# Optimization experiments

Hardware: AMD Instinct MI355X
Metric: run time of the kernel (lower is better)

The kernel has to match this reference:

```python
import jax, jax.numpy as jnp
import numpy as np

M_DIM = 1024
N_HEADS = 16
H_DIM = M_DIM // N_HEADS
FFN_H = 2 * M_DIM
B, S = 2, 2048
EPS = 1e-5
NEG = -1e9


def layernorm(x, g, b):
    mu = jnp.mean(x, axis=-1, keepdims=True)
    var = jnp.mean((x - mu) ** 2, axis=-1, keepdims=True)
    return (x - mu) * jax.lax.rsqrt(var + EPS) * g + b


def setup_inputs() -> dict:
    key = jax.random.key(0)
    ks = jax.random.split(key, 16)
    sc = 0.02
    return {
        "x": jax.random.normal(ks[0], (B, S, M_DIM), jnp.float32),
        "attention_mask": jnp.ones((B, S), jnp.int32),
        # per-head QKV projections stacked over heads: [H, M, D]
        "Wq": jax.random.normal(ks[1], (N_HEADS, M_DIM, H_DIM), jnp.float32) * sc,
        "bq": jnp.zeros((N_HEADS, H_DIM), jnp.float32),
        "Wk": jax.random.normal(ks[2], (N_HEADS, M_DIM, H_DIM), jnp.float32) * sc,
        "bk": jnp.zeros((N_HEADS, H_DIM), jnp.float32),
        "Wv": jax.random.normal(ks[3], (N_HEADS, M_DIM, H_DIM), jnp.float32) * sc,
        "bv": jnp.zeros((N_HEADS, H_DIM), jnp.float32),
        "Wo": jax.random.normal(ks[4], (M_DIM, M_DIM), jnp.float32) * sc,
        "bo": jnp.zeros((M_DIM,), jnp.float32),
        "g1": jnp.ones((M_DIM,), jnp.float32),
        "b1": jnp.zeros((M_DIM,), jnp.float32),
        "W1": jax.random.normal(ks[5], (M_DIM, FFN_H), jnp.float32) * sc,
        "bias1": jnp.zeros((FFN_H,), jnp.float32),
        "W2": jax.random.normal(ks[6], (FFN_H, M_DIM), jnp.float32) * sc,
        "bias2": jnp.zeros((M_DIM,), jnp.float32),
        "g2": jnp.ones((M_DIM,), jnp.float32),
        "b2": jnp.zeros((M_DIM,), jnp.float32),
    }


def reference(x, attention_mask, Wq, bq, Wk, bk, Wv, bv, Wo, bo, g1, b1, W1, bias1, W2, bias2, g2, b2):
    # All heads at once (the torch code loops over heads; same math).
    q = jnp.einsum("bsm,hmd->bhsd", x, Wq) + bq[None, :, None, :]
    k = jnp.einsum("bsm,hmd->bhsd", x, Wk) + bk[None, :, None, :]
    v = jnp.einsum("bsm,hmd->bhsd", x, Wv) + bv[None, :, None, :]
    scores = jnp.einsum("bhqd,bhkd->bhqk", q, k) / jnp.sqrt(jnp.float32(H_DIM))
    mask = attention_mask[:, None, None, :].astype(bool)  # [B,1,1,S] over keys
    scores = jnp.where(mask, scores, NEG)
    attn = jax.nn.softmax(scores, axis=-1)
    ctx = jnp.einsum("bhqk,bhkd->bhqd", attn, v)
    ctx = ctx.transpose(0, 2, 1, 3).reshape(x.shape[0], x.shape[1], M_DIM)  # concat heads
    out = ctx @ Wo + bo
    out = layernorm(out + x, g1, b1)
    fout = jax.nn.relu(out @ W1 + bias1) @ W2 + bias2
    out = layernorm(out + fout, g2, b2)
    return out
```

## Files before the change

### kernel.cpp

```cpp
#include <hip/hip_runtime.h>

#define MDIM 1024
#define FFH  2048
#define SEQ  2048
#define AST  72
#define VST  136
#define QSCL 0.18033688f

#if __has_builtin(__builtin_amdgcn_exp2f)
  #define EXP2(x) __builtin_amdgcn_exp2f(x)
#else
  #define EXP2(x) exp2f(x)
#endif

typedef __attribute__((ext_vector_type(8))) __bf16 bf16x8;
typedef __attribute__((ext_vector_type(4))) float floatx4;
typedef __attribute__((ext_vector_type(8))) unsigned short ushort8;
typedef __attribute__((address_space(3))) unsigned int lds_uint;
typedef const __attribute__((address_space(1))) unsigned int g_uint;

__device__ __forceinline__ unsigned short f2bf(float f){
  union { float f; unsigned u; } v; v.f = f;
  unsigned u = v.u;
  u += 0x7fffu + ((u >> 16) & 1u);
  return (unsigned short)(u >> 16);
}
__device__ __forceinline__ unsigned short f2bf_tr(float f){
  union { float f; unsigned u; } v; v.f = f;
  return (unsigned short)(v.u >> 16);
}

__global__ void k_cvt_qb(const float* __restrict__ x, unsigned short* __restrict__ xb,
                         const float* __restrict__ bq, const float* __restrict__ bk,
                         const float* __restrict__ bv, float* __restrict__ qbias){
  const int bid = blockIdx.x, t = threadIdx.x;
  if (bid < 4096){
    int i = (bid * 256 + t) * 4;
    float4 v = *(const float4*)(x + i);
    ushort4 o;
    o.x = f2bf(v.x); o.y = f2bf(v.y); o.z = f2bf(v.z); o.w = f2bf(v.w);
    *(ushort4*)(xb + i) = o;
  } else {
    int i = (bid - 4096) * 256 + t;
    qbias[i] = (i < 1024) ? bq[i] * QSCL : (i < 2048) ? bk[i - 1024] : bv[i - 2048];
  }
}

__global__ void __launch_bounds__(256) k_prep_w(const float* __restrict__ Wo, const float* __restrict__ W1,
                                                const float* __restrict__ W2, const float* __restrict__ Wq,
                                                const float* __restrict__ Wk, const float* __restrict__ Wv,
                                                unsigned short* __restrict__ wot, unsigned short* __restrict__ w1t,
                                                unsigned short* __restrict__ w2t, unsigned short* __restrict__ wqkvt){
  __shared__ unsigned short Ts[32 * 36];
  const int t = threadIdx.x, bid = blockIdx.x;
  const int lr = t >> 3, lc4 = (t & 7) << 2;
  if (bid >= 5120){
    const int id = bid - 5120;
    const int xm = id & 31, yd = (id >> 5) & 1, z = id >> 6;
    const int tensor = z >> 4, h = z & 15;
    const float* W = (tensor == 0) ? Wq : (tensor == 1) ? Wk : Wv;
    const float scl = (tensor == 0) ? QSCL : 1.0f;
    const int m0 = xm << 5, d0 = yd << 5;
    float4 v = *(const float4*)(W + ((size_t)h << 16) + (size_t)(m0 + lr) * 64 + d0 + lc4);
    ushort4 o; o.x = f2bf(v.x * scl); o.y = f2bf(v.y * scl); o.z = f2bf(v.z * scl); o.w = f2bf(v.w * scl);
    *(ushort4*)&Ts[lr * 36 + lc4] = o;
    __syncthreads();
    ushort4 w;
    w.x = Ts[(lc4 + 0) * 36 + lr];
    w.y = Ts[(lc4 + 1) * 36 + lr];
    w.z = Ts[(lc4 + 2) * 36 + lr];
    w.w = Ts[(lc4 + 3) * 36 + lr];
    const int n = (tensor << 10) + (h << 6) + d0 + lr;
    *(ushort4*)(wqkvt + ((size_t)n << 10) + m0 + lc4) = w;
    return;
  }
  const float* src; unsigned short* dst; int K, N, k0, n0;
  if (bid < 1024){
    src = Wo; dst = wot; K = 1024; N = 1024;
    n0 = (bid & 31) << 5; k0 = (bid >> 5) << 5;
  } else if (bid < 3072){
    const int id = bid - 1024;
    src = W1; dst = w1t; K = 1024; N = 2048;
    n0 = (id & 63) << 5; k0 = (id >> 6) << 5;
  } else {
    const int id = bid - 3072;
    src = W2; dst = w2t; K = 2048; N = 1024;
    n0 = (id & 31) << 5; k0 = (id >> 5) << 5;
  }
  float4 v = *(const float4*)(src + (size_t)(k0 + lr) * N + n0 + lc4);
  ushort4 o; o.x = f2bf(v.x); o.y = f2bf(v.y); o.z = f2bf(v.z); o.w = f2bf(v.w);
  *(ushort4*)&Ts[lr * 36 + lc4] = o;
  __syncthreads();
  ushort4 w;
  w.x = Ts[(lc4 + 0) * 36 + lr];
  w.y = Ts[(lc4 + 1) * 36 + lr];
  w.z = Ts[(lc4 + 2) * 36 + lr];
  w.w = Ts[(lc4 + 3) * 36 + lr];
  *(ushort4*)(dst + (size_t)(n0 + lr) * K + k0 + lc4) = w;
}

template<int RELU, int OUTBF>
__global__ void __launch_bounds__(256) k_gemm128(const unsigned short* __restrict__ A,
                                                 const unsigned short* __restrict__ Bt,
                                                 const float* __restrict__ bias,
                                                 void* __restrict__ Cout, int N, int K){
  __shared__ unsigned short As[2 * 128 * 32];
  __shared__ unsigned short Bs[2 * 128 * 32];
  const int t = threadIdx.x;
  const int m0 = blockIdx.y << 7, n0 = blockIdx.x << 7;
  const int lane = t & 63, w = t >> 6;
  const int quad = lane >> 4, l16 = lane & 15;
  const int mw = (w & 1) << 6, nw = (w >> 1) << 6;
  floatx4 acc[4][4];
  #pragma unroll
  for (int i = 0; i < 4; i++)
    #pragma unroll
    for (int j = 0; j < 4; j++) acc[i][j] = (floatx4){0.f, 0.f, 0.f, 0.f};
  const unsigned short* Ag  = A  + (size_t)(m0 + (t >> 2)) * K + ((t & 3) << 3);
  const unsigned short* Ag2 = Ag + (size_t)64 * K;
  const unsigned short* Bg  = Bt + (size_t)(n0 + (t >> 2)) * K + ((t & 3) << 3);
  const unsigned short* Bg2 = Bg + (size_t)64 * K;
  for (int kb = 0; kb < K; kb += 64){
    #pragma unroll
    for (int s = 0; s < 2; s++){
      const int ko = kb + (s << 5), lo = (s << 12) + (t << 3);
      __builtin_amdgcn_global_load_lds((g_uint*)(Ag  + ko), (lds_uint*)&As[lo],        16, 0, 0);
      __builtin_amdgcn_global_load_lds((g_uint*)(Ag2 + ko), (lds_uint*)&As[lo + 2048], 16, 0, 0);
      __builtin_amdgcn_global_load_lds((g_uint*)(Bg  + ko), (lds_uint*)&Bs[lo],        16, 0, 0);
      __builtin_amdgcn_global_load_lds((g_uint*)(Bg2 + ko), (lds_uint*)&Bs[lo + 2048], 16, 0, 0);
    }
    __syncthreads();
    #pragma unroll
    for (int s = 0; s < 2; s++){
      const int sb = s << 12;
      bf16x8 af[4], bf[4];
      #pragma unroll
      for (int mt = 0; mt < 4; mt++)
        af[mt] = *(const bf16x8*)&As[sb + ((mw + (mt << 4) + l16) << 5) + (quad << 3)];
      #pragma unroll
      for (int nt = 0; nt < 4; nt++)
        bf[nt] = *(const bf16x8*)&Bs[sb + ((nw + (nt << 4) + l16) << 5) + (quad << 3)];
      #pragma unroll
      for (int mt = 0; mt < 4; mt++)
        #pragma unroll
        for (int nt = 0; nt < 4; nt++)
          acc[mt][nt] = __builtin_amdgcn_mfma_f32_16x16x32_bf16(af[mt], bf[nt], acc[mt][nt], 0, 0, 0);
    }
    __syncthreads();
  }
  #pragma unroll
  for (int nt = 0; nt < 4; nt++){
    const int col = n0 + nw + (nt << 4) + l16;
    const float bsv = bias[col];
    #pragma unroll
    for (int mt = 0; mt < 4; mt++){
      const int row = m0 + mw + (mt << 4) + (quad << 2);
      #pragma unroll
      for (int r = 0; r < 4; r++){
        float v = acc[mt][nt][r] + bsv;
        if (RELU) v = fmaxf(v, 0.f);
        if (OUTBF) ((unsigned short*)Cout)[(size_t)(row + r) * N + col] = f2bf(v);
        else       ((float*)Cout)[(size_t)(row + r) * N + col] = v;
      }
    }
  }
}

template<int RELU, int OUTBF>
__global__ void __launch_bounds__(256) k_gemm64n(const unsigned short* __restrict__ A,
                                                 const unsigned short* __restrict__ Bt,
                                                 const float* __restrict__ bias,
                                                 void* __restrict__ Cout, int N, int K){
  __shared__ unsigned short As[2 * 128 * 32];
  __shared__ unsigned short Bs[2 * 64 * 32];
  const int t = threadIdx.x;
  const int m0 = blockIdx.y << 7, n0 = blockIdx.x << 6;
  const int lane = t & 63, w = t >> 6;
  const int quad = lane >> 4, l16 = lane & 15;
  const int mw = (w & 1) << 6, nw = (w >> 1) << 5;
  floatx4 acc[4][2];
  #pragma unroll
  for (int i = 0; i < 4; i++)
    #pragma unroll
    for (int j = 0; j < 2; j++) acc[i][j] = (floatx4){0.f, 0.f, 0.f, 0.f};
  const unsigned short* Ag  = A  + (size_t)(m0 + (t >> 2)) * K + ((t & 3) << 3);
  const unsigned short* Ag2 = Ag + (size_t)64 * K;
  const unsigned short* Bg  = Bt + (size_t)(n0 + (t >> 2)) * K + ((t & 3) << 3);
  for (int kb = 0; kb < K; kb += 64){
    #pragma unroll
    for (int s = 0; s < 2; s++){
      const int ko = kb + (s << 5);
      __builtin_amdgcn_global_load_lds((g_uint*)(Ag  + ko), (lds_uint*)&As[(s << 12) + (t << 3)],        16, 0, 0);
      __builtin_amdgcn_global_load_lds((g_uint*)(Ag2 + ko), (lds_uint*)&As[(s << 12) + (t << 3) + 2048], 16, 0, 0);
      __builtin_amdgcn_global_load_lds((g_uint*)(Bg  + ko), (lds_uint*)&Bs[(s << 11) + (t << 3)],        16, 0, 0);
    }
    __syncthreads();
    #pragma unroll
    for (int s = 0; s < 2; s++){
      bf16x8 af[4], bf[2];
      #pragma unroll
      for (int mt = 0; mt < 4; mt++)
        af[mt] = *(const bf16x8*)&As[(s << 12) + ((mw + (mt << 4) + l16) << 5) + (quad << 3)];
      #pragma unroll
      for (int nt = 0; nt < 2; nt++)
        bf[nt] = *(const bf16x8*)&Bs[(s << 11) + ((nw + (nt << 4) + l16) << 5) + (quad << 3)];
      #pragma unroll
      for (int mt = 0; mt < 4; mt++)
        #pragma unroll
        for (int nt = 0; nt < 2; nt++)
          acc[mt][nt] = __builtin_amdgcn_mfma_f32_16x16x32_bf16(af[mt], bf[nt], acc[mt][nt], 0, 0, 0);
    }
    __syncthreads();
  }
  #pragma unroll
  for (int nt = 0; nt < 2; nt++){
    const int col = n0 + nw + (nt << 4) + l16;
    const float bsv = bias[col];
    #pragma unroll
    for (int mt = 0; mt < 4; mt++){
      const int row = m0 + mw + (mt << 4) + (quad << 2);
      #pragma unroll
      for (int r = 0; r < 4; r++){
        float v = acc[mt][nt][r] + bsv;
        if (RELU) v = fmaxf(v, 0.f);
        if (OUTBF) ((unsigned short*)Cout)[(size_t)(row + r) * N + col] = f2bf(v);
        else       ((float*)Cout)[(size_t)(row + r) * N + col] = v;
      }
    }
  }
}

__global__ void __launch_bounds__(256, 2) k_attn(const unsigned short* __restrict__ qkvb,
                                                 const int* __restrict__ amask,
                                                 unsigned short* __restrict__ ctxb){
  __shared__ __align__(16) unsigned short Ks[2][128 * AST];
  __shared__ __align__(16) unsigned short Vt[2][64 * VST];
  __shared__ __align__(16) int msk[2][128];
  const int t = threadIdx.x;
  const int w = t >> 6, lane = t & 63;
  const int quad = lane >> 4, l16 = lane & 15;
  const int b = blockIdx.y >> 4, h = blockIdx.y & 15;
  const int q0 = blockIdx.x << 7;
  const int r0 = (w << 5) + l16;
  const int r1 = r0 + 16;
  const int sr = t >> 2, sc = (t & 3) << 4;
  const int kg = t >> 4, dc = (t & 15) << 2;
  const int swz  = (dc >> 4) & 3;
  const int pc0  = ((((kg & 3) | ((kg >> 3) << 2)) ^ swz) << 3) | (((kg >> 2) & 1) << 2);

  {
    const int qr = t >> 1, qc = (t & 1) << 5;
    const unsigned short* qs = qkvb + (size_t)((b << 11) + q0 + qr) * 3072 + (h << 6) + qc;
    unsigned short* qd = &Ks[0][qr * AST + qc];
    *(uint4*)(qd)      = *(const uint4*)(qs);
    *(uint4*)(qd + 8)  = *(const uint4*)(qs + 8);
    *(uint4*)(qd + 16) = *(const uint4*)(qs + 16);
    *(uint4*)(qd + 24) = *(const uint4*)(qs + 24);
  }
  __syncthreads();
  const bf16x8 qa0 = *(const bf16x8*)&Ks[0][r0 * AST + (quad << 3)];
  const bf16x8 qa1 = *(const bf16x8*)&Ks[0][r0 * AST + (quad << 3) + 32];
  const bf16x8 qb0 = *(const bf16x8*)&Ks[0][r1 * AST + (quad << 3)];
  const bf16x8 qb1 = *(const bf16x8*)&Ks[0][r1 * AST + (quad << 3) + 32];

  floatx4 accA[4], accB[4];
  #pragma unroll
  for (int i = 0; i < 4; i++){
    accA[i] = (floatx4){0.f, 0.f, 0.f, 0.f};
    accB[i] = (floatx4){0.f, 0.f, 0.f, 0.f};
  }
  float l_runA = 0.f, l_runB = 0.f;

  const unsigned short* kbase  = qkvb + (size_t)((b << 11) + sr) * 3072 + 1024 + (h << 6) + sc;
  const unsigned short* kbase2 = kbase + (size_t)64 * 3072;
  const unsigned short* vbase  = qkvb + (size_t)((b << 11) + (kg << 2)) * 3072 + 2048 + (h << 6) + dc;
  const unsigned short* vbase2 = vbase + (size_t)64 * 3072;
  const int* mbase = amask + (b << 11);

  uint4 krA, krB, krC, krD;
  ushort4 va0, va1, va2, va3, vb0, vb1, vb2, vb3;
  int mreg = 1;

#define LOADT(tt) { \
    const size_t off = (size_t)((tt) << 7) * 3072; \
    krA = *(const uint4*)(kbase + off); \
    krB = *(const uint4*)(kbase + off + 8); \
    krC = *(const uint4*)(kbase2 + off); \
    krD = *(const uint4*)(kbase2 + off + 8); \
    va0 = *(const ushort4*)(vbase + off); \
    va1 = *(const ushort4*)(vbase + off + 3072); \
    va2 = *(const ushort4*)(vbase + off + 2 * 3072); \
    va3 = *(const ushort4*)(vbase + off + 3 * 3072); \
    vb0 = *(const ushort4*)(vbase2 + off); \
    vb1 = *(const ushort4*)(vbase2 + off + 3072); \
    vb2 = *(const ushort4*)(vbase2 + off + 2 * 3072); \
    vb3 = *(const ushort4*)(vbase2 + off + 3 * 3072); \
    if (t < 128) mreg = mbase[((tt) << 7) + t]; \
  }

#define STORET(dst) { \
    unsigned short* Kd = Ks[dst]; \
    unsigned short* Vd = Vt[dst]; \
    *(uint4*)&Kd[sr * AST + sc]            = krA; \
    *(uint4*)&Kd[sr * AST + sc + 8]        = krB; \
    *(uint4*)&Kd[(sr + 64) * AST + sc]     = krC; \
    *(uint4*)&Kd[(sr + 64) * AST + sc + 8] = krD; \
    ushort4 cc; \
    cc.x = va0.x; cc.y = va1.x; cc.z = va2.x; cc.w = va3.x; *(ushort4*)&Vd[(dc + 0) * VST + pc0] = cc; \
    cc.x = va0.y; cc.y = va1.y; cc.z = va2.y; cc.w = va3.y; *(ushort4*)&Vd[(dc + 1) * VST + pc0] = cc; \
    cc.x = va0.z; cc.y = va1.z; cc.z = va2.z; cc.w = va3.z; *(ushort4*)&Vd[(dc + 2) * VST + pc0] = cc; \
    cc.x = va0.w; cc.y = va1.w; cc.z = va2.w; cc.w = va3.w; *(ushort4*)&Vd[(dc + 3) * VST + pc0] = cc; \
    cc.x = vb0.x; cc.y = vb1.x; cc.z = vb2.x; cc.w = vb3.x; *(ushort4*)&Vd[(dc + 0) * VST + pc0 + 64] = cc; \
    cc.x = vb0.y; cc.y = vb1.y; cc.z = vb2.y; cc.w = vb3.y; *(ushort4*)&Vd[(dc + 1) * VST + pc0 + 64] = cc; \
    cc.x = vb0.z; cc.y = vb1.z; cc.z = vb2.z; cc.w = vb3.z; *(ushort4*)&Vd[(dc + 2) * VST + pc0 + 64] = cc; \
    cc.x = vb0.w; cc.y = vb1.w; cc.z = vb2.w; cc.w = vb3.w; *(ushort4*)&Vd[(dc + 3) * VST + pc0 + 64] = cc; \
    if (t < 128) msk[dst][t] = mreg; \
  }

  LOADT(0);
  __syncthreads();
  STORET(0);
  LOADT(1);
  __syncthreads();

  int c = 0;
  for (int kt = 0; kt < 16; kt++){
    if (kt + 1 < 16) STORET(c ^ 1);
    if (kt + 2 < 16) LOADT(kt + 2);
    {
      const unsigned short* Kc = Ks[c];
      const unsigned short* Vc = Vt[c];
      const int* Mc = msk[c];
      float lsA = 0.f, lsB = 0.f;
      #pragma unroll
      for (int s = 0; s < 4; s++){
        const unsigned short* kp = &Kc[((s << 5) + l16) * AST + (quad << 3)];
        const bf16x8 k00 = *(const bf16x8*)(kp);
        const bf16x8 k01 = *(const bf16x8*)(kp + 32);
        const bf16x8 k10 = *(const bf16x8*)(kp + (AST << 4));
        const bf16x8 k11 = *(const bf16x8*)(kp + (AST << 4) + 32);
        floatx4 sA0 = (floatx4){0.f, 0.f, 0.f, 0.f};
        floatx4 sB0 = (floatx4){0.f, 0.f, 0.f, 0.f};
        floatx4 sA1 = (floatx4){0.f, 0.f, 0.f, 0.f};
        floatx4 sB1 = (floatx4){0.f, 0.f, 0.f, 0.f};
        __builtin_amdgcn_s_setprio(1);
        sA0 = __builtin_amdgcn_mfma_f32_16x16x32_bf16(k00, qa0, sA0, 0, 0, 0);
        sA0 = __builtin_amdgcn_mfma_f32_16x16x32_bf16(k01, qa1, sA0, 0, 0, 0);
        sB0 = __builtin_amdgcn_mfma_f32_16x16x32_bf16(k00, qb0, sB0, 0, 0, 0);
        sB0 = __builtin_amdgcn_mfma_f32_16x16x32_bf16(k01, qb1, sB0, 0, 0, 0);
        sA1 = __builtin_amdgcn_mfma_f32_16x16x32_bf16(k10, qa0, sA1, 0, 0, 0);
        sA1 = __builtin_amdgcn_mfma_f32_16x16x32_bf16(k11, qa1, sA1, 0, 0, 0);
        sB1 = __builtin_amdgcn_mfma_f32_16x16x32_bf16(k10, qb0, sB1, 0, 0, 0);
        sB1 = __builtin_amdgcn_mfma_f32_16x16x32_bf16(k11, qb1, sB1, 0, 0, 0);
        __builtin_amdgcn_s_setprio(0);
        const int4 m0 = *(const int4*)&Mc[(s << 5) + (quad << 2)];
        const int4 m1 = *(const int4*)&Mc[(s << 5) + 16 + (quad << 2)];
        const float a0 = m0.x ? EXP2(sA0[0]) : 0.f;
        const float a1 = m0.y ? EXP2(sA0[1]) : 0.f;
        const float a2 = m0.z ? EXP2(sA0[2]) : 0.f;
        const float a3 = m0.w ? EXP2(sA0[3]) : 0.f;
        const float a4 = m1.x ? EXP2(sA1[0]) : 0.f;
        const float a5 = m1.y ? EXP2(sA1[1]) : 0.f;
        const float a6 = m1.z ? EXP2(sA1[2]) : 0.f;
        const float a7 = m1.w ? EXP2(sA1[3]) : 0.f;
        const float b0 = m0.x ? EXP2(sB0[0]) : 0.f;
        const float b1 = m0.y ? EXP2(sB0[1]) : 0.f;
        const float b2 = m0.z ? EXP2(sB0[2]) : 0.f;
        const float b3 = m0.w ? EXP2(sB0[3]) : 0.f;
        const float b4 = m1.x ? EXP2(sB1[0]) : 0.f;
        const float b5 = m1.y ? EXP2(sB1[1]) : 0.f;
        const float b6 = m1.z ? EXP2(sB1[2]) : 0.f;
        const float b7 = m1.w ? EXP2(sB1[3]) : 0.f;
        lsA += (a0 + a1) + (a2 + a3) + (a4 + a5) + (a6 + a7);
        lsB += (b0 + b1) + (b2 + b3) + (b4 + b5) + (b6 + b7);
        ushort8 uA, uB;
        uA[0] = f2bf_tr(a0); uA[1] = f2bf_tr(a1); uA[2] = f2bf_tr(a2); uA[3] = f2bf_tr(a3);
        uA[4] = f2bf_tr(a4); uA[5] = f2bf_tr(a5); uA[6] = f2bf_tr(a6); uA[7] = f2bf_tr(a7);
        uB[0] = f2bf_tr(b0); uB[1] = f2bf_tr(b1); uB[2] = f2bf_tr(b2); uB[3] = f2bf_tr(b3);
        uB[4] = f2bf_tr(b4); uB[5] = f2bf_tr(b5); uB[6] = f2bf_tr(b6); uB[7] = f2bf_tr(b7);
        const bf16x8 pfA = __builtin_bit_cast(bf16x8, uA);
        const bf16x8 pfB = __builtin_bit_cast(bf16x8, uB);
        __builtin_amdgcn_s_setprio(1);
        #pragma unroll
        for (int mt = 0; mt < 4; mt++){
          const bf16x8 vf = *(const bf16x8*)&Vc[((mt << 4) + l16) * VST + ((((s << 2) + quad) ^ mt) << 3)];
          accA[mt] = __builtin_amdgcn_mfma_f32_16x16x32_bf16(vf, pfA, accA[mt], 0, 0, 0);
          accB[mt] = __builtin_amdgcn_mfma_f32_16x16x32_bf16(vf, pfB, accB[mt], 0, 0, 0);
        }
        __builtin_amdgcn_s_setprio(0);
      }
      l_runA += lsA;
      l_runB += lsB;
    }
    __syncthreads();
    c ^= 1;
  }
#undef LOADT
#undef STORET

  l_runA += __shfl_xor(l_runA, 16);
  l_runA += __shfl_xor(l_runA, 32);
  l_runB += __shfl_xor(l_runB, 16);
  l_runB += __shfl_xor(l_runB, 32);
  const float liA = 1.f / l_runA;
  const float liB = 1.f / l_runB;
  unsigned short* oA = ctxb + (size_t)((b << 11) + q0 + r0) * 1024 + (h << 6);
  unsigned short* oB = ctxb + (size_t)((b << 11) + q0 + r1) * 1024 + (h << 6);
  #pragma unroll
  for (int mt = 0; mt < 4; mt++){
    ushort4 o;
    o.x = f2bf(accA[mt][0] * liA);
    o.y = f2bf(accA[mt][1] * liA);
    o.z = f2bf(accA[mt][2] * liA);
    o.w = f2bf(accA[mt][3] * liA);
    *(ushort4*)&oA[(mt << 4) + (quad << 2)] = o;
    o.x = f2bf(accB[mt][0] * liB);
    o.y = f2bf(accB[mt][1] * liB);
    o.z = f2bf(accB[mt][2] * liB);
    o.w = f2bf(accB[mt][3] * liB);
    *(ushort4*)&oB[(mt << 4) + (quad << 2)] = o;
  }
}

__global__ void __launch_bounds__(256) k_ln(const unsigned short* __restrict__ a,
                                            const float* __restrict__ res,
                                            const float* __restrict__ gg, const float* __restrict__ bb,
                                            float* __restrict__ out, unsigned short* __restrict__ outb){
  const int row = blockIdx.x, t = threadIdx.x;
  const ushort4 au = ((const ushort4*)(a + (size_t)row * 1024))[t];
  const float4 rv = ((const float4*)(res + (size_t)row * 1024))[t];
  float4 v;
  { union { unsigned u; float f; } c;
    c.u = (unsigned)au.x << 16; v.x = c.f + rv.x;
    c.u = (unsigned)au.y << 16; v.y = c.f + rv.y;
    c.u = (unsigned)au.z << 16; v.z = c.f + rv.z;
    c.u = (unsigned)au.w << 16; v.w = c.f + rv.w; }
  float sum = v.x + v.y + v.z + v.w;
  float ss  = v.x * v.x + v.y * v.y + v.z * v.z + v.w * v.w;
  #pragma unroll
  for (int off = 32; off > 0; off >>= 1){
    sum += __shfl_down(sum, off);
    ss  += __shfl_down(ss, off);
  }
  __shared__ float red[8];
  const int w = t >> 6;
  if ((t & 63) == 0){ red[w] = sum; red[4 + w] = ss; }
  __syncthreads();
  const float S  = red[0] + red[1] + red[2] + red[3];
  const float SS = red[4] + red[5] + red[6] + red[7];
  const float mu  = S * (1.f / 1024.f);
  const float var = SS * (1.f / 1024.f) - mu * mu;
  const float rs  = rsqrtf(var + 1e-5f);
  const float4 gv = ((const float4*)gg)[t];
  const float4 bv = ((const float4*)bb)[t];
  float4 o;
  o.x = (v.x - mu) * rs * gv.x + bv.x;
  o.y = (v.y - mu) * rs * gv.y + bv.y;
  o.z = (v.z - mu) * rs * gv.z + bv.z;
  o.w = (v.w - mu) * rs * gv.w + bv.w;
  ((float4*)(out + (size_t)row * 1024))[t] = o;
  if (outb){
    ushort4 ob; ob.x = f2bf(o.x); ob.y = f2bf(o.y); ob.z = f2bf(o.z); ob.w = f2bf(o.w);
    ((ushort4*)(outb + (size_t)row * 1024))[t] = ob;
  }
}

extern "C" void kernel_launch(void* const* d_in, const int* in_sizes, int n_in,
                              void* d_out, int out_size, void* d_ws, size_t ws_size,
                              hipStream_t stream){
  const float* x     = (const float*)d_in[0];
  const int*   amask = (const int*)d_in[1];
  const float* Wq    = (const float*)d_in[2];
  const float* bq    = (const float*)d_in[3];
  const float* Wk    = (const float*)d_in[4];
  const float* bk    = (const float*)d_in[5];
  const float* Wv    = (const float*)d_in[6];
  const float* bv    = (const float*)d_in[7];
  const float* Wo    = (const float*)d_in[8];
  const float* bo    = (const float*)d_in[9];
  const float* g1    = (const float*)d_in[10];
  const float* b1    = (const float*)d_in[11];
  const float* W1    = (const float*)d_in[12];
  const float* bias1 = (const float*)d_in[13];
  const float* W2    = (const float*)d_in[14];
  const float* bias2 = (const float*)d_in[15];
  const float* g2    = (const float*)d_in[16];
  const float* b2    = (const float*)d_in[17];

  char* ws = (char*)d_ws;
  unsigned short* xb    = (unsigned short*)(ws + 0);
  unsigned short* wqkvt = (unsigned short*)(ws + 8388608);
  float*          qbias = (float*)         (ws + 14680064);
  unsigned short* wot   = (unsigned short*)(ws + 14692352);
  unsigned short* w1t   = (unsigned short*)(ws + 16789504);
  unsigned short* w2t   = (unsigned short*)(ws + 20983808);
  unsigned short* ctxb  = (unsigned short*)(ws + 25178112);
  unsigned short* attnb = (unsigned short*)(ws + 33566720);
  unsigned short* fbufb = attnb;
  unsigned short* qkvb  = (unsigned short*)(ws + 50343936);
  float*          out1  = (float*)         (ws + 50343936);
  unsigned short* out1b = (unsigned short*)(ws + 50343936 + 25165824);
  unsigned short* h1    = (unsigned short*)(ws + 50343936 + 33554432);

  k_cvt_qb<<<dim3(4108), dim3(256), 0, stream>>>(x, xb, bq, bk, bv, qbias);
  k_prep_w<<<dim3(8192), dim3(256), 0, stream>>>(Wo, W1, W2, Wq, Wk, Wv, wot, w1t, w2t, wqkvt);

  k_gemm128<0,1><<<dim3(24, 32), dim3(256), 0, stream>>>(xb, wqkvt, qbias, qkvb, 3072, 1024);
  k_attn<<<dim3(16, 32), dim3(256), 0, stream>>>(qkvb, amask, ctxb);
  k_gemm64n<0,1><<<dim3(16, 32), dim3(256), 0, stream>>>(ctxb, wot, bo, attnb, MDIM, 1024);
  k_ln<<<dim3(4096), dim3(256), 0, stream>>>(attnb, x, g1, b1, out1, out1b);
  k_gemm128<1,1><<<dim3(16, 32), dim3(256), 0, stream>>>(out1b, w1t, bias1, h1, FFH, 1024);
  k_gemm64n<0,1><<<dim3(16, 32), dim3(256), 0, stream>>>(h1, w2t, bias2, fbufb, MDIM, 2048);
  k_ln<<<dim3(4096), dim3(256), 0, stream>>>(fbufb, out1, g2, b2, (float*)d_out, nullptr);
}
```

Baseline: 312.6 us.

## Double-buffer LDS tiles in bf16 GEMM kernels to overlap loads with MFMA

Both GEMM kernels (128x128 and 128x64 tiles) now use two LDS buffers. The next K-tile's global_load_lds is issued into the spare buffer before the MFMA work on the current buffer, with one barrier per iteration. The aim is to hide global-to-LDS latency behind matrix math instead of stalling on it each step. In exchange, per-block LDS use doubles, which can cut the number of resident blocks per CU.

```diff
diff --git a/kernel.cpp b/kernel.cpp
--- a/kernel.cpp
+++ b/kernel.cpp
@@ -104,8 +104,8 @@
                                                  const unsigned short* __restrict__ Bt,
                                                  const float* __restrict__ bias,
                                                  void* __restrict__ Cout, int N, int K){
-  __shared__ unsigned short As[2 * 128 * 32];
-  __shared__ unsigned short Bs[2 * 128 * 32];
+  __shared__ unsigned short As[2][2 * 128 * 32];
+  __shared__ unsigned short Bs[2][2 * 128 * 32];
   const int t = threadIdx.x;
   const int m0 = blockIdx.y << 7, n0 = blockIdx.x << 7;
   const int lane = t & 63, w = t >> 6;
@@ -120,26 +120,34 @@
   const unsigned short* Ag2 = Ag + (size_t)64 * K;
   const unsigned short* Bg  = Bt + (size_t)(n0 + (t >> 2)) * K + ((t & 3) << 3);
   const unsigned short* Bg2 = Bg + (size_t)64 * K;
+
+#define STG128(Ad, Bd, kb) { \
+    _Pragma("unroll") \
+    for (int s = 0; s < 2; s++){ \
+      const int ko = (kb) + (s << 5), lo = (s << 12) + (t << 3); \
+      __builtin_amdgcn_global_load_lds((g_uint*)(Ag  + ko), (lds_uint*)&(Ad)[lo],        16, 0, 0); \
+      __builtin_amdgcn_global_load_lds((g_uint*)(Ag2 + ko), (lds_uint*)&(Ad)[lo + 2048], 16, 0, 0); \
+      __builtin_amdgcn_global_load_lds((g_uint*)(Bg  + ko), (lds_uint*)&(Bd)[lo],        16, 0, 0); \
+      __builtin_amdgcn_global_load_lds((g_uint*)(Bg2 + ko), (lds_uint*)&(Bd)[lo + 2048], 16, 0, 0); \
+    } }
+
+  STG128(As[0], Bs[0], 0);
+  __syncthreads();
+  int cur = 0;
   for (int kb = 0; kb < K; kb += 64){
-    #pragma unroll
-    for (int s = 0; s < 2; s++){
-      const int ko = kb + (s << 5), lo = (s << 12) + (t << 3);
-      __builtin_amdgcn_global_load_lds((g_uint*)(Ag  + ko), (lds_uint*)&As[lo],        16, 0, 0);
-      __builtin_amdgcn_global_load_lds((g_uint*)(Ag2 + ko), (lds_uint*)&As[lo + 2048], 16, 0, 0);
-      __builtin_amdgcn_global_load_lds((g_uint*)(Bg  + ko), (lds_uint*)&Bs[lo],        16, 0, 0);
-      __builtin_amdgcn_global_load_lds((g_uint*)(Bg2 + ko), (lds_uint*)&Bs[lo + 2048], 16, 0, 0);
-    }
-    __syncthreads();
+    if (kb + 64 < K) STG128(As[cur ^ 1], Bs[cur ^ 1], kb + 64);
+    const unsigned short* Ar = As[cur];
+    const unsigned short* Br = Bs[cur];
     #pragma unroll
     for (int s = 0; s < 2; s++){
       const int sb = s << 12;
       bf16x8 af[4], bf[4];
       #pragma unroll
       for (int mt = 0; mt < 4; mt++)
-        af[mt] = *(const bf16x8*)&As[sb + ((mw + (mt << 4) + l16) << 5) + (quad << 3)];
+        af[mt] = *(const bf16x8*)&Ar[sb + ((mw + (mt << 4) + l16) << 5) + (quad << 3)];
       #pragma unroll
       for (int nt = 0; nt < 4; nt++)
-        bf[nt] = *(const bf16x8*)&Bs[sb + ((nw + (nt << 4) + l16) << 5) + (quad << 3)];
+        bf[nt] = *(const bf16x8*)&Br[sb + ((nw + (nt << 4) + l16) << 5) + (quad << 3)];
       #pragma unroll
       for (int mt = 0; mt < 4; mt++)
         #pragma unroll
@@ -147,7 +155,9 @@
           acc[mt][nt] = __builtin_amdgcn_mfma_f32_16x16x32_bf16(af[mt], bf[nt], acc[mt][nt], 0, 0, 0);
     }
     __syncthreads();
-  }
+    cur ^= 1;
+  }
+#undef STG128
   #pragma unroll
   for (int nt = 0; nt < 4; nt++){
     const int col = n0 + nw + (nt << 4) + l16;
@@ -171,8 +181,8 @@
                                                  const unsigned short* __restrict__ Bt,
                                                  const float* __restrict__ bias,
                                                  void* __restrict__ Cout, int N, int K){
-  __shared__ unsigned short As[2 * 128 * 32];
-  __shared__ unsigned short Bs[2 * 64 * 32];
+  __shared__ unsigned short As[2][2 * 128 * 32];
+  __shared__ unsigned short Bs[2][2 * 64 * 32];
   const int t = threadIdx.x;
   const int m0 = blockIdx.y << 7, n0 = blockIdx.x << 6;
   const int lane = t & 63, w = t >> 6;
@@ -186,24 +196,32 @@
   const unsigned short* Ag  = A  + (size_t)(m0 + (t >> 2)) * K + ((t & 3) << 3);
   const unsigned short* Ag2 = Ag + (size_t)64 * K;
   const unsigned short* Bg  = Bt + (size_t)(n0 + (t >> 2)) * K + ((t & 3) << 3);
+
+#define STG64(Ad, Bd, kb) { \
+    _Pragma("unroll") \
+    for (int s = 0; s < 2; s++){ \
+      const int ko = (kb) + (s << 5); \
+      __builtin_amdgcn_global_load_lds((g_uint*)(Ag  + ko), (lds_uint*)&(Ad)[(s << 12) + (t << 3)],        16, 0, 0); \
+      __builtin_amdgcn_global_load_lds((g_uint*)(Ag2 + ko), (lds_uint*)&(Ad)[(s << 12) + (t << 3) + 2048], 16, 0, 0); \
+      __builtin_amdgcn_global_load_lds((g_uint*)(Bg  + ko), (lds_uint*)&(Bd)[(s << 11) + (t << 3)],        16, 0, 0); \
+    } }
+
+  STG64(As[0], Bs[0], 0);
+  __syncthreads();
+  int cur = 0;
   for (int kb = 0; kb < K; kb += 64){
-    #pragma unroll
-    for (int s = 0; s < 2; s++){
-      const int ko = kb + (s << 5);
-      __builtin_amdgcn_global_load_lds((g_uint*)(Ag  + ko), (lds_uint*)&As[(s << 12) + (t << 3)],        16, 0, 0);
-      __builtin_amdgcn_global_load_lds((g_uint*)(Ag2 + ko), (lds_uint*)&As[(s << 12) + (t << 3) + 2048], 16, 0, 0);
-      __builtin_amdgcn_global_load_lds((g_uint*)(Bg  + ko), (lds_uint*)&Bs[(s << 11) + (t << 3)],        16, 0, 0);
-    }
-    __syncthreads();
+    if (kb + 64 < K) STG64(As[cur ^ 1], Bs[cur ^ 1], kb + 64);
+    const unsigned short* Ar = As[cur];
+    const unsigned short* Br = Bs[cur];
     #pragma unroll
     for (int s = 0; s < 2; s++){
       bf16x8 af[4], bf[2];
       #pragma unroll
       for (int mt = 0; mt < 4; mt++)
-        af[mt] = *(const bf16x8*)&As[(s << 12) + ((mw + (mt << 4) + l16) << 5) + (quad << 3)];
+        af[mt] = *(const bf16x8*)&Ar[(s << 12) + ((mw + (mt << 4) + l16) << 5) + (quad << 3)];
       #pragma unroll
       for (int nt = 0; nt < 2; nt++)
-        bf[nt] = *(const bf16x8*)&Bs[(s << 11) + ((nw + (nt << 4) + l16) << 5) + (quad << 3)];
+        bf[nt] = *(const bf16x8*)&Br[(s << 11) + ((nw + (nt << 4) + l16) << 5) + (quad << 3)];
       #pragma unroll
       for (int mt = 0; mt < 4; mt++)
         #pragma unroll
@@ -211,7 +229,9 @@
           acc[mt][nt] = __builtin_amdgcn_mfma_f32_16x16x32_bf16(af[mt], bf[nt], acc[mt][nt], 0, 0, 0);
     }
     __syncthreads();
-  }
+    cur ^= 1;
+  }
+#undef STG64
   #pragma unroll
   for (int nt = 0; nt < 2; nt++){
     const int col = n0 + nw + (nt << 4) + l16;
```

Result: faster. 303.8 us (-2.8%).
